# Kernel optimization log

Hardware: AMD Instinct MI355X
Metric: run time of the kernel (lower is better)

The kernel has to match this reference:

```python
import jax, jax.numpy as jnp
import numpy as np

N_NODES = 50000
NEG_SLOPE = 0.2  # PyG GATConv default leaky-relu slope


def _gat_conv(x, edge_index, W, a_src, a_dst, bias, heads, out_ch, concat, num_nodes):
    # x: [N, F_in]; W: [F_in, heads*out_ch]; a_src/a_dst: [heads, out_ch]; bias: [heads*out_ch] or [out_ch]
    h = (x @ W).reshape(num_nodes, heads, out_ch)            # [N,H,C]
    alpha_src = jnp.einsum('nhc,hc->nh', h, a_src)           # [N,H]
    alpha_dst = jnp.einsum('nhc,hc->nh', h, a_dst)           # [N,H]
    src, dst = edge_index[0], edge_index[1]
    e = jax.nn.leaky_relu(alpha_src[src] + alpha_dst[dst], NEG_SLOPE)  # [E,H]
    # segment softmax over incoming edges per destination (self-loops guarantee non-empty segments)
    m = jax.ops.segment_max(e, dst, num_segments=num_nodes)
    e = jnp.exp(e - m[dst])
    denom = jax.ops.segment_sum(e, dst, num_segments=num_nodes)
    alpha = e / denom[dst]                                    # [E,H]
    msg = h[src] * alpha[:, :, None]                          # [E,H,C]
    out = jax.ops.segment_sum(msg, dst, num_segments=num_nodes)  # [N,H,C]
    if concat:
        out = out.reshape(num_nodes, heads * out_ch)
    else:
        out = out.mean(axis=1)
    return out + bias


def _add_self_loops(edge_index, num_nodes):
    loops = jnp.arange(num_nodes, dtype=edge_index.dtype)
    return jnp.concatenate([edge_index, jnp.stack([loops, loops])], axis=1)


def setup_inputs() -> dict:
    key = jax.random.key(0)
    ks = jax.random.split(key, 16)
    N, F_in, H, C_hid, C_out = N_NODES, 128, 4, 64, 64
    E = 800000
    x = jax.random.normal(ks[0], (N, F_in), dtype=jnp.float32)
    edge_index = jax.random.randint(ks[1], (2, E), 0, N, dtype=jnp.int32)
    s = lambda fan: 1.0 / np.sqrt(fan)
    inp = {
        'x': x, 'edge_index': edge_index,
        'W1': jax.random.normal(ks[2], (F_in, H * C_hid), jnp.float32) * s(F_in),
        'a_src1': jax.random.normal(ks[3], (H, C_hid), jnp.float32) * s(C_hid),
        'a_dst1': jax.random.normal(ks[4], (H, C_hid), jnp.float32) * s(C_hid),
        'b1': jnp.zeros((H * C_hid,), jnp.float32),
        'W2': jax.random.normal(ks[5], (H * C_hid, H * C_hid), jnp.float32) * s(H * C_hid),
        'a_src2': jax.random.normal(ks[6], (H, C_hid), jnp.float32) * s(C_hid),
        'a_dst2': jax.random.normal(ks[7], (H, C_hid), jnp.float32) * s(C_hid),
        'b2': jnp.zeros((H * C_hid,), jnp.float32),
        'W3': jax.random.normal(ks[8], (H * C_hid, C_out), jnp.float32) * s(H * C_hid),
        'a_src3': jax.random.normal(ks[9], (1, C_out), jnp.float32) * s(C_out),
        'a_dst3': jax.random.normal(ks[10], (1, C_out), jnp.float32) * s(C_out),
        'b3': jnp.zeros((C_out,), jnp.float32),
    }
    return inp


def reference(x, edge_index, W1, a_src1, a_dst1, b1, W2, a_src2, a_dst2, b2, W3, a_src3, a_dst3, b3):
    N = x.shape[0]
    ei = _add_self_loops(edge_index, N)
    h = _gat_conv(x, ei, W1, a_src1, a_dst1, b1, heads=4, out_ch=64, concat=True, num_nodes=N)
    h = jax.nn.elu(h)
    h = _gat_conv(h, ei, W2, a_src2, a_dst2, b2, heads=4, out_ch=64, concat=True, num_nodes=N)
    h = jax.nn.elu(h)
    out = _gat_conv(h, ei, W3, a_src3, a_dst3, b3, heads=1, out_ch=64, concat=False, num_nodes=N)
    return out
```

## Files before the change

### kernel.cpp

```cpp
#include <hip/hip_runtime.h>
#include <hip/hip_fp16.h>
#include <cstdint>


typedef _Float16 f16;
typedef _Float16 f16x8 __attribute__((ext_vector_type(8)));
typedef float f32x4 __attribute__((ext_vector_type(4)));

__global__ __launch_bounds__(256) void count_kernel(const int* __restrict__ ei,
                                                    int E, int N,
                                                    int* __restrict__ deg) {
  int g = blockIdx.x * 256 + threadIdx.x;
  if (g >= E + N) return;
  int dst = (g < E) ? ei[E + g] : (g - E);
  atomicAdd(&deg[dst], 1);
}

__global__ __launch_bounds__(256) void deg_block_reduce(const int* __restrict__ deg,
                                                        int* __restrict__ bsum, int N) {
  __shared__ int red[4];
  int b = blockIdx.x;
  int v = 0;
#pragma unroll
  for (int s = 0; s < 4; ++s) {
    int idx = b * 1024 + s * 256 + threadIdx.x;
    if (idx < N) v += deg[idx];
  }
  for (int off = 32; off; off >>= 1) v += __shfl_down(v, off);
  if ((threadIdx.x & 63) == 0) red[threadIdx.x >> 6] = v;
  __syncthreads();
  if (threadIdx.x == 0) bsum[b] = red[0] + red[1] + red[2] + red[3];
}

__global__ __launch_bounds__(1024) void small_scan(const int* __restrict__ bsum,
                                                   int* __restrict__ bpre, int NB) {
  __shared__ int buf[1024];
  int v = (threadIdx.x < NB) ? bsum[threadIdx.x] : 0;
  buf[threadIdx.x] = v;
  __syncthreads();
  for (int off = 1; off < 1024; off <<= 1) {
    int tv = (threadIdx.x >= off) ? buf[threadIdx.x - off] : 0;
    __syncthreads();
    buf[threadIdx.x] += tv;
    __syncthreads();
  }
  if (threadIdx.x < NB) bpre[threadIdx.x] = buf[threadIdx.x] - v;
}

__global__ __launch_bounds__(1024) void scan_final(const int* __restrict__ deg,
                                                   const int* __restrict__ bpre,
                                                   int* __restrict__ row_off,
                                                   int* __restrict__ cursor,
                                                   int N, int total) {
  __shared__ int buf[1024];
  int b = blockIdx.x;
  int i = b * 1024 + threadIdx.x;
  int v = (i < N) ? deg[i] : 0;
  buf[threadIdx.x] = v;
  __syncthreads();
  for (int off = 1; off < 1024; off <<= 1) {
    int tv = (threadIdx.x >= off) ? buf[threadIdx.x - off] : 0;
    __syncthreads();
    buf[threadIdx.x] += tv;
    __syncthreads();
  }
  if (i < N) {
    int ro = bpre[b] + buf[threadIdx.x] - v;
    row_off[i] = ro;
    cursor[i] = ro;
  }
  if (i == 0) row_off[N] = total;
}

__global__ __launch_bounds__(256) void scatter_kernel(const int* __restrict__ ei,
                                                      int E, int N,
                                                      int* __restrict__ cursor,
                                                      int* __restrict__ esrc,
                                                      int* __restrict__ edst) {
  int g = blockIdx.x * 256 + threadIdx.x;
  if (g >= E + N) return;
  int src, dst;
  if (g < E) { src = ei[g]; dst = ei[E + g]; }
  else       { src = g - E; dst = src; }
  int pos = atomicAdd(&cursor[dst], 1);
  esrc[pos] = src;
  edst[pos] = dst;
}

__global__ __launch_bounds__(256) void convert_x(const float* __restrict__ x,
                                                 f16* __restrict__ xh, int n) {
  int i = (blockIdx.x * 256 + threadIdx.x) * 4;
  if (i >= n) return;
  float4 v = *reinterpret_cast<const float4*>(&x[i]);
  f16 o[4] = {(f16)v.x, (f16)v.y, (f16)v.z, (f16)v.w};
  *reinterpret_cast<uint2*>(&xh[i]) = *reinterpret_cast<uint2*>(o);
}

__global__ __launch_bounds__(256) void convert_wt(const float* __restrict__ W,
                                                  f16* __restrict__ Wt,
                                                  int K, int Ncol) {
  int t = blockIdx.x * 256 + threadIdx.x;
  if (t >= K * Ncol) return;
  int n = t % Ncol, k = t / Ncol;
  Wt[(size_t)n * K + k] = (f16)W[t];
}

template <int BN>
__global__ __launch_bounds__(256) void mfma_gemm_alpha(
    const f16* __restrict__ A,
    const f16* __restrict__ Bt,
    f16* __restrict__ Tout,
    const float* __restrict__ avec_src, const float* __restrict__ avec_dst,
    float* __restrict__ asrc, float* __restrict__ adst,
    int M, int K, int Ncol) {
  constexpr int CF = BN / 16;
  constexpr int HL = BN / 64;
  __shared__ f16 As[128][40];
  __shared__ f16 Bs[BN][40];
  int tid = threadIdx.x;
  int wv = tid >> 6, lane = tid & 63;
  int lrow = lane & 15, lkb = lane >> 4;
  int row0 = blockIdx.x * 128, col0 = blockIdx.y * BN;

  f32x4 acc[2][CF];
#pragma unroll
  for (int rf = 0; rf < 2; ++rf)
#pragma unroll
    for (int cf = 0; cf < CF; ++cf) acc[rf][cf] = (f32x4){0.f, 0.f, 0.f, 0.f};

  for (int kk = 0; kk < K; kk += 32) {
#pragma unroll
    for (int q = 0; q < 2; ++q) {
      int slot = tid + q * 256;
      int r = slot >> 2, ko = (slot & 3) << 3;
      int gr = min(row0 + r, M - 1);
      *reinterpret_cast<f16x8*>(&As[r][ko]) =
          *reinterpret_cast<const f16x8*>(&A[(size_t)gr * K + kk + ko]);
    }
#pragma unroll
    for (int q = 0; q < BN / 64; ++q) {
      int slot = tid + q * 256;
      int c = slot >> 2, ko = (slot & 3) << 3;
      *reinterpret_cast<f16x8*>(&Bs[c][ko]) =
          *reinterpret_cast<const f16x8*>(&Bt[(size_t)(col0 + c) * K + kk + ko]);
    }
    __syncthreads();
    f16x8 af[2], bf[CF];
#pragma unroll
    for (int rf = 0; rf < 2; ++rf)
      af[rf] = *reinterpret_cast<f16x8*>(&As[wv * 32 + rf * 16 + lrow][lkb * 8]);
#pragma unroll
    for (int cf = 0; cf < CF; ++cf)
      bf[cf] = *reinterpret_cast<f16x8*>(&Bs[cf * 16 + lrow][lkb * 8]);
#pragma unroll
    for (int rf = 0; rf < 2; ++rf)
#pragma unroll
      for (int cf = 0; cf < CF; ++cf)
        acc[rf][cf] = __builtin_amdgcn_mfma_f32_16x16x32_f16(af[rf], bf[cf],
                                                             acc[rf][cf], 0, 0, 0);
    __syncthreads();
  }

  int Hh = Ncol >> 6;
  float avs[HL][4], avd[HL][4];
#pragma unroll
  for (int hl = 0; hl < HL; ++hl) {
    int hg = (col0 >> 6) + hl;
#pragma unroll
    for (int q = 0; q < 4; ++q) {
      avs[hl][q] = avec_src[hg * 64 + q * 16 + lrow];
      avd[hl][q] = avec_dst[hg * 64 + q * 16 + lrow];
    }
  }

#pragma unroll
  for (int rf = 0; rf < 2; ++rf) {
#pragma unroll
    for (int hl = 0; hl < HL; ++hl) {
      int hg = (col0 >> 6) + hl;
#pragma unroll
      for (int r = 0; r < 4; ++r) {
        float ps = 0.f, pd = 0.f;
#pragma unroll
        for (int q = 0; q < 4; ++q) {
          float v = acc[rf][hl * 4 + q][r];
          ps = fmaf(v, avs[hl][q], ps);
          pd = fmaf(v, avd[hl][q], pd);
        }
#pragma unroll
        for (int off = 1; off < 16; off <<= 1) {
          ps += __shfl_xor(ps, off);
          pd += __shfl_xor(pd, off);
        }
        int row = row0 + wv * 32 + rf * 16 + lkb * 4 + r;
        if (lrow == 0 && row < M) {
          asrc[row * Hh + hg] = ps;
          adst[row * Hh + hg] = pd;
        }
      }
    }
#pragma unroll
    for (int r = 0; r < 4; ++r) {
      int row = row0 + wv * 32 + rf * 16 + lkb * 4 + r;
      if (row < M) {
#pragma unroll
        for (int cf = 0; cf < CF; ++cf)
          Tout[(size_t)row * Ncol + col0 + cf * 16 + lrow] = (f16)acc[rf][cf][r];
      }
    }
  }
}

__global__ __launch_bounds__(256) void edge_weights_h4(
    const int* __restrict__ esrc, const int* __restrict__ edst,
    const float* __restrict__ asrc, const float* __restrict__ adst,
    float* __restrict__ w, int ET) {
  int t = blockIdx.x * 256 + threadIdx.x;
  if (t >= ET * 4) return;
  int j = t >> 2, h = t & 3;
  float e = asrc[esrc[j] * 4 + h] + adst[edst[j] * 4 + h];
  e = fmaxf(e, 0.2f * e);
  w[t] = __expf(e);
}

__global__ __launch_bounds__(256) void edge_weights_h1(
    const int* __restrict__ esrc, const int* __restrict__ edst,
    const float* __restrict__ asrc, const float* __restrict__ adst,
    float* __restrict__ w, int ET) {
  int j = blockIdx.x * 256 + threadIdx.x;
  if (j >= ET) return;
  float e = asrc[esrc[j]] + adst[edst[j]];
  e = fmaxf(e, 0.2f * e);
  w[j] = __expf(e);
}

template <bool ELU>
__global__ __launch_bounds__(256) void aggregate_h4(
    const f16* __restrict__ T16, const int* __restrict__ row_off,
    const int* __restrict__ esrc, const float* __restrict__ w,
    const float* __restrict__ bias, f16* __restrict__ outF, int N) {
  int wv = threadIdx.x >> 6, lane = threadIdx.x & 63;
  int dst = blockIdx.x * 4 + wv;
  if (dst >= N) return;
  int head = lane >> 4;
  int r0 = row_off[dst], r1 = row_off[dst + 1];
  const char* tbase = reinterpret_cast<const char*>(T16);
  uint loff = (uint)lane * 8;
  float den = 0.f, ax = 0.f, ay = 0.f, az = 0.f, aw = 0.f;
#pragma unroll 2
  for (int j = r0; j < r1; ++j) {
    int sj = esrc[j];
    float wj = w[(j << 2) + head];
    den += wj;
    uint2 raw = *reinterpret_cast<const uint2*>(tbase + (((uint)sj << 9) + loff));
    __half2 p0 = *reinterpret_cast<__half2*>(&raw.x);
    __half2 p1 = *reinterpret_cast<__half2*>(&raw.y);
    float2 f0 = __half22float2(p0);
    float2 f1 = __half22float2(p1);
    ax = fmaf(wj, f0.x, ax);
    ay = fmaf(wj, f0.y, ay);
    az = fmaf(wj, f1.x, az);
    aw = fmaf(wj, f1.y, aw);
  }
  float rd = 1.f / den;
  float4 bv = *reinterpret_cast<const float4*>(&bias[lane << 2]);
  float vx = ax * rd + bv.x, vy = ay * rd + bv.y;
  float vz = az * rd + bv.z, vw = aw * rd + bv.w;
  if (ELU) {
    vx = vx > 0.f ? vx : expm1f(vx);
    vy = vy > 0.f ? vy : expm1f(vy);
    vz = vz > 0.f ? vz : expm1f(vz);
    vw = vw > 0.f ? vw : expm1f(vw);
  }
  f16 o[4] = {(f16)vx, (f16)vy, (f16)vz, (f16)vw};
  *reinterpret_cast<uint2*>(&outF[(size_t)dst * 256 + (lane << 2)]) =
      *reinterpret_cast<uint2*>(o);
}

__global__ __launch_bounds__(256) void aggregate_h1(
    const f16* __restrict__ T16, const int* __restrict__ row_off,
    const int* __restrict__ esrc, const float* __restrict__ w,
    const float* __restrict__ bias, float* __restrict__ out, int N) {
  int wv = threadIdx.x >> 6, lane = threadIdx.x & 63;
  int g = lane >> 4, l = lane & 15;
  int dst = blockIdx.x * 4 + wv;
  if (dst >= N) return;
  int r0 = row_off[dst], r1 = row_off[dst + 1];
  const char* tbase = reinterpret_cast<const char*>(T16);
  uint coff = (uint)l * 8;
  float den = 0.f, ax = 0.f, ay = 0.f, az = 0.f, aw = 0.f;
#pragma unroll 2
  for (int j = r0 + g; j < r1; j += 4) {
    int sj = esrc[j];
    float wj = w[j];
    den += wj;
    uint2 raw = *reinterpret_cast<const uint2*>(tbase + (((uint)sj << 7) + coff));
    __half2 p0 = *reinterpret_cast<__half2*>(&raw.x);
    __half2 p1 = *reinterpret_cast<__half2*>(&raw.y);
    float2 f0 = __half22float2(p0);
    float2 f1 = __half22float2(p1);
    ax = fmaf(wj, f0.x, ax);
    ay = fmaf(wj, f0.y, ay);
    az = fmaf(wj, f1.x, az);
    aw = fmaf(wj, f1.y, aw);
  }
#pragma unroll
  for (int off = 16; off < 64; off <<= 1) {
    ax += __shfl_xor(ax, off);
    ay += __shfl_xor(ay, off);
    az += __shfl_xor(az, off);
    aw += __shfl_xor(aw, off);
    den += __shfl_xor(den, off);
  }
  if (lane < 16) {
    float rd = 1.f / den;
    float4 v;
    v.x = ax * rd + bias[l * 4 + 0];
    v.y = ay * rd + bias[l * 4 + 1];
    v.z = az * rd + bias[l * 4 + 2];
    v.w = aw * rd + bias[l * 4 + 3];
    *reinterpret_cast<float4*>(&out[(size_t)dst * 64 + l * 4]) = v;
  }
}

extern "C" void kernel_launch(void* const* d_in, const int* in_sizes, int n_in,
                              void* d_out, int out_size, void* d_ws, size_t ws_size,
                              hipStream_t stream) {
  const float* x   = (const float*)d_in[0];
  const int*   ei  = (const int*)d_in[1];
  const float* W1  = (const float*)d_in[2];
  const float* as1 = (const float*)d_in[3];
  const float* ad1 = (const float*)d_in[4];
  const float* b1  = (const float*)d_in[5];
  const float* W2  = (const float*)d_in[6];
  const float* as2 = (const float*)d_in[7];
  const float* ad2 = (const float*)d_in[8];
  const float* b2  = (const float*)d_in[9];
  const float* W3  = (const float*)d_in[10];
  const float* as3 = (const float*)d_in[11];
  const float* ad3 = (const float*)d_in[12];
  const float* b3  = (const float*)d_in[13];
  float* out = (float*)d_out;

  const int Fin = 128, H = 4, C = 64, HC = H * C;
  const int N = in_sizes[0] / Fin;
  const int E = in_sizes[1] / 2;
  const int ET = E + N;
  const int NB = (N + 1023) / 1024;

  f16* xh    = (f16*)d_ws;
  f16* T16   = xh + (size_t)N * Fin;
  f16* F16   = T16 + (size_t)N * HC;
  f16* T16L3 = F16 + (size_t)N * HC;
  f16* Wt1   = T16L3 + (size_t)N * C;
  f16* Wt2   = Wt1 + HC * Fin;
  f16* Wt3   = Wt2 + HC * HC;
  float* asrc = (float*)(Wt3 + C * HC);
  float* adst = asrc + (size_t)N * H;
  float* wbuf = adst + (size_t)N * H;
  int* deg     = (int*)(wbuf + (size_t)ET * 4);
  int* row_off = deg + N;
  int* cursor  = row_off + (N + 1);
  int* bsum    = cursor + N;
  int* bpre    = bsum + NB;
  int* esrc    = bpre + NB;
  int* edst    = esrc + ET;

  hipMemsetAsync(deg, 0, N * sizeof(int), stream);
  count_kernel<<<(ET + 255) / 256, 256, 0, stream>>>(ei, E, N, deg);
  deg_block_reduce<<<NB, 256, 0, stream>>>(deg, bsum, N);
  small_scan<<<1, 1024, 0, stream>>>(bsum, bpre, NB);
  scan_final<<<NB, 1024, 0, stream>>>(deg, bpre, row_off, cursor, N, ET);
  scatter_kernel<<<(ET + 255) / 256, 256, 0, stream>>>(ei, E, N, cursor, esrc, edst);

  convert_x<<<(N * Fin / 4 + 255) / 256, 256, 0, stream>>>(x, xh, N * Fin);
  convert_wt<<<(Fin * HC + 255) / 256, 256, 0, stream>>>(W1, Wt1, Fin, HC);
  convert_wt<<<(HC * HC + 255) / 256, 256, 0, stream>>>(W2, Wt2, HC, HC);
  convert_wt<<<(HC * C + 255) / 256, 256, 0, stream>>>(W3, Wt3, HC, C);

  int gx = (N + 127) / 128;
  int eb4 = (ET * 4 + 255) / 256, eb1 = (ET + 255) / 256;
  int ab = (N + 3) / 4;

  mfma_gemm_alpha<128><<<dim3(gx, 2), 256, 0, stream>>>(
      xh, Wt1, T16, as1, ad1, asrc, adst, N, Fin, HC);
  edge_weights_h4<<<eb4, 256, 0, stream>>>(esrc, edst, asrc, adst, wbuf, ET);
  aggregate_h4<true><<<ab, 256, 0, stream>>>(T16, row_off, esrc, wbuf, b1, F16, N);

  mfma_gemm_alpha<128><<<dim3(gx, 2), 256, 0, stream>>>(
      F16, Wt2, T16, as2, ad2, asrc, adst, N, HC, HC);
  edge_weights_h4<<<eb4, 256, 0, stream>>>(esrc, edst, asrc, adst, wbuf, ET);
  aggregate_h4<true><<<ab, 256, 0, stream>>>(T16, row_off, esrc, wbuf, b2, F16, N);

  mfma_gemm_alpha<64><<<dim3(gx, 1), 256, 0, stream>>>(
      F16, Wt3, T16L3, as3, ad3, asrc, adst, N, HC, C);
  edge_weights_h1<<<eb1, 256, 0, stream>>>(esrc, edst, asrc, adst, wbuf, ET);
  aggregate_h1<<<ab, 256, 0, stream>>>(T16L3, row_off, esrc, wbuf, b3, out, N);
}
```

Before: 367.2 us.

## Slice feature matrices into 32-column panels and aggregate per slice

GEMM outputs and aggregation outputs now use a column-sliced layout: 32-wide f16 panels, each stored contiguously over all nodes. The aggregation kernel runs one block per slice and node chunk, with 8 lanes per edge row and 8 edges in flight per wave. The aim is a smaller gather footprint per pass so it stays in L2/cache, plus more memory-level parallelism per destination. Edge weights are computed once per edge with float4 loads and stored head-major. The cost is that edge indices and weights are re-read once per slice, adding index traffic.

New measurement: 518.0 us. +41.1%, slower.

```diff
diff --git a/kernel.cpp b/kernel.cpp
--- a/kernel.cpp
+++ b/kernel.cpp
@@ -105,10 +105,9 @@
   Wt[(size_t)n * K + k] = (f16)W[t];
 }
 
-template <int BN>
+template <int BN, bool ASL>
 __global__ __launch_bounds__(256) void mfma_gemm_alpha(
-    const f16* __restrict__ A,
-    const f16* __restrict__ Bt,
+    const f16* __restrict__ A, const f16* __restrict__ Bt,
     f16* __restrict__ Tout,
     const float* __restrict__ avec_src, const float* __restrict__ avec_dst,
     float* __restrict__ asrc, float* __restrict__ adst,
@@ -121,6 +120,7 @@
   int wv = tid >> 6, lane = tid & 63;
   int lrow = lane & 15, lkb = lane >> 4;
   int row0 = blockIdx.x * 128, col0 = blockIdx.y * BN;
+  size_t Msl = (size_t)M * 32;
 
   f32x4 acc[2][CF];
 #pragma unroll
@@ -134,8 +134,9 @@
       int slot = tid + q * 256;
       int r = slot >> 2, ko = (slot & 3) << 3;
       int gr = min(row0 + r, M - 1);
-      *reinterpret_cast<f16x8*>(&As[r][ko]) =
-          *reinterpret_cast<const f16x8*>(&A[(size_t)gr * K + kk + ko]);
+      const f16* Ap = ASL ? &A[(size_t)(kk >> 5) * Msl + (size_t)gr * 32 + ko]
+                          : &A[(size_t)gr * K + kk + ko];
+      *reinterpret_cast<f16x8*>(&As[r][ko]) = *reinterpret_cast<const f16x8*>(Ap);
     }
 #pragma unroll
     for (int q = 0; q < BN / 64; ++q) {
@@ -204,8 +205,11 @@
       int row = row0 + wv * 32 + rf * 16 + lkb * 4 + r;
       if (row < M) {
 #pragma unroll
-        for (int cf = 0; cf < CF; ++cf)
-          Tout[(size_t)row * Ncol + col0 + cf * 16 + lrow] = (f16)acc[rf][cf][r];
+        for (int cf = 0; cf < CF; ++cf) {
+          int col = col0 + cf * 16 + lrow;
+          Tout[(size_t)(col >> 5) * Msl + (size_t)row * 32 + (col & 31)] =
+              (f16)acc[rf][cf][r];
+        }
       }
     }
   }
@@ -215,12 +219,18 @@
     const int* __restrict__ esrc, const int* __restrict__ edst,
     const float* __restrict__ asrc, const float* __restrict__ adst,
     float* __restrict__ w, int ET) {
-  int t = blockIdx.x * 256 + threadIdx.x;
-  if (t >= ET * 4) return;
-  int j = t >> 2, h = t & 3;
-  float e = asrc[esrc[j] * 4 + h] + adst[edst[j] * 4 + h];
-  e = fmaxf(e, 0.2f * e);
-  w[t] = __expf(e);
+  int j = blockIdx.x * 256 + threadIdx.x;
+  if (j >= ET) return;
+  float4 s4 = *reinterpret_cast<const float4*>(&asrc[esrc[j] * 4]);
+  float4 d4 = *reinterpret_cast<const float4*>(&adst[edst[j] * 4]);
+  float e0 = s4.x + d4.x; e0 = fmaxf(e0, 0.2f * e0);
+  float e1 = s4.y + d4.y; e1 = fmaxf(e1, 0.2f * e1);
+  float e2 = s4.z + d4.z; e2 = fmaxf(e2, 0.2f * e2);
+  float e3 = s4.w + d4.w; e3 = fmaxf(e3, 0.2f * e3);
+  w[j] = __expf(e0);
+  w[ET + j] = __expf(e1);
+  w[2 * ET + j] = __expf(e2);
+  w[3 * ET + j] = __expf(e3);
 }
 
 __global__ __launch_bounds__(256) void edge_weights_h1(
@@ -234,92 +244,70 @@
   w[j] = __expf(e);
 }
 
-template <bool ELU>
-__global__ __launch_bounds__(256) void aggregate_h4(
-    const f16* __restrict__ T16, const int* __restrict__ row_off,
-    const int* __restrict__ esrc, const float* __restrict__ w,
-    const float* __restrict__ bias, f16* __restrict__ outF, int N) {
+template <int NSL, bool ELU, bool F32OUT>
+__global__ __launch_bounds__(256) void aggregate_sliced(
+    const f16* __restrict__ Tsl,
+    const int* __restrict__ row_off, const int* __restrict__ esrc,
+    const float* __restrict__ w,
+    const float* __restrict__ bias, void* __restrict__ outp,
+    int N, int ET) {
+  int s = blockIdx.x % NSL;
+  int chunk = blockIdx.x / NSL;
   int wv = threadIdx.x >> 6, lane = threadIdx.x & 63;
-  int dst = blockIdx.x * 4 + wv;
-  if (dst >= N) return;
-  int head = lane >> 4;
-  int r0 = row_off[dst], r1 = row_off[dst + 1];
-  const char* tbase = reinterpret_cast<const char*>(T16);
-  uint loff = (uint)lane * 8;
-  float den = 0.f, ax = 0.f, ay = 0.f, az = 0.f, aw = 0.f;
-#pragma unroll 2
-  for (int j = r0; j < r1; ++j) {
-    int sj = esrc[j];
-    float wj = w[(j << 2) + head];
-    den += wj;
-    uint2 raw = *reinterpret_cast<const uint2*>(tbase + (((uint)sj << 9) + loff));
-    __half2 p0 = *reinterpret_cast<__half2*>(&raw.x);
-    __half2 p1 = *reinterpret_cast<__half2*>(&raw.y);
-    float2 f0 = __half22float2(p0);
-    float2 f1 = __half22float2(p1);
-    ax = fmaf(wj, f0.x, ax);
-    ay = fmaf(wj, f0.y, ay);
-    az = fmaf(wj, f1.x, az);
-    aw = fmaf(wj, f1.y, aw);
-  }
-  float rd = 1.f / den;
-  float4 bv = *reinterpret_cast<const float4*>(&bias[lane << 2]);
-  float vx = ax * rd + bv.x, vy = ay * rd + bv.y;
-  float vz = az * rd + bv.z, vw = aw * rd + bv.w;
-  if (ELU) {
-    vx = vx > 0.f ? vx : expm1f(vx);
-    vy = vy > 0.f ? vy : expm1f(vy);
-    vz = vz > 0.f ? vz : expm1f(vz);
-    vw = vw > 0.f ? vw : expm1f(vw);
-  }
-  f16 o[4] = {(f16)vx, (f16)vy, (f16)vz, (f16)vw};
-  *reinterpret_cast<uint2*>(&outF[(size_t)dst * 256 + (lane << 2)]) =
-      *reinterpret_cast<uint2*>(o);
-}
-
-__global__ __launch_bounds__(256) void aggregate_h1(
-    const f16* __restrict__ T16, const int* __restrict__ row_off,
-    const int* __restrict__ esrc, const float* __restrict__ w,
-    const float* __restrict__ bias, float* __restrict__ out, int N) {
-  int wv = threadIdx.x >> 6, lane = threadIdx.x & 63;
-  int g = lane >> 4, l = lane & 15;
-  int dst = blockIdx.x * 4 + wv;
-  if (dst >= N) return;
-  int r0 = row_off[dst], r1 = row_off[dst + 1];
-  const char* tbase = reinterpret_cast<const char*>(T16);
-  uint coff = (uint)l * 8;
-  float den = 0.f, ax = 0.f, ay = 0.f, az = 0.f, aw = 0.f;
-#pragma unroll 2
-  for (int j = r0 + g; j < r1; j += 4) {
-    int sj = esrc[j];
-    float wj = w[j];
-    den += wj;
-    uint2 raw = *reinterpret_cast<const uint2*>(tbase + (((uint)sj << 7) + coff));
-    __half2 p0 = *reinterpret_cast<__half2*>(&raw.x);
-    __half2 p1 = *reinterpret_cast<__half2*>(&raw.y);
-    float2 f0 = __half22float2(p0);
-    float2 f1 = __half22float2(p1);
-    ax = fmaf(wj, f0.x, ax);
-    ay = fmaf(wj, f0.y, ay);
-    az = fmaf(wj, f1.x, az);
-    aw = fmaf(wj, f1.y, aw);
-  }
-#pragma unroll
-  for (int off = 16; off < 64; off <<= 1) {
-    ax += __shfl_xor(ax, off);
-    ay += __shfl_xor(ay, off);
-    az += __shfl_xor(az, off);
-    aw += __shfl_xor(aw, off);
-    den += __shfl_xor(den, off);
-  }
-  if (lane < 16) {
-    float rd = 1.f / den;
-    float4 v;
-    v.x = ax * rd + bias[l * 4 + 0];
-    v.y = ay * rd + bias[l * 4 + 1];
-    v.z = az * rd + bias[l * 4 + 2];
-    v.w = aw * rd + bias[l * 4 + 3];
-    *reinterpret_cast<float4*>(&out[(size_t)dst * 64 + l * 4]) = v;
+  int g = lane >> 3, l = lane & 7;
+  int head = s >> 1;
+  const f16* tb = Tsl + (size_t)s * N * 32;
+  const float* wh = w + (size_t)head * ET;
+  int dbase = chunk * 16 + wv * 4;
+#pragma unroll
+  for (int d = 0; d < 4; ++d) {
+    int dst = dbase + d;
+    if (dst >= N) return;
+    int r0 = row_off[dst], r1 = row_off[dst + 1];
+    float den = 0.f, ax = 0.f, ay = 0.f, az = 0.f, aw = 0.f;
+    for (int j = r0 + g; j < r1; j += 8) {
+      int sj = esrc[j];
+      float wj = wh[j];
+      den += wj;
+      uint2 raw = *reinterpret_cast<const uint2*>(tb + (size_t)sj * 32 + l * 4);
+      __half2 p0 = *reinterpret_cast<__half2*>(&raw.x);
+      __half2 p1 = *reinterpret_cast<__half2*>(&raw.y);
+      float2 f0 = __half22float2(p0);
+      float2 f1 = __half22float2(p1);
+      ax = fmaf(wj, f0.x, ax);
+      ay = fmaf(wj, f0.y, ay);
+      az = fmaf(wj, f1.x, az);
+      aw = fmaf(wj, f1.y, aw);
+    }
+#pragma unroll
+    for (int off = 8; off < 64; off <<= 1) {
+      ax += __shfl_xor(ax, off);
+      ay += __shfl_xor(ay, off);
+      az += __shfl_xor(az, off);
+      aw += __shfl_xor(aw, off);
+      den += __shfl_xor(den, off);
+    }
+    if (lane < 8) {
+      float rd = 1.f / den;
+      int c0 = s * 32 + l * 4;
+      float4 bv = *reinterpret_cast<const float4*>(&bias[c0]);
+      float vx = ax * rd + bv.x, vy = ay * rd + bv.y;
+      float vz = az * rd + bv.z, vw = aw * rd + bv.w;
+      if (ELU) {
+        vx = vx > 0.f ? vx : expm1f(vx);
+        vy = vy > 0.f ? vy : expm1f(vy);
+        vz = vz > 0.f ? vz : expm1f(vz);
+        vw = vw > 0.f ? vw : expm1f(vw);
+      }
+      if (F32OUT) {
+        *reinterpret_cast<float4*>((float*)outp + (size_t)dst * (NSL * 32) + c0) =
+            make_float4(vx, vy, vz, vw);
+      } else {
+        f16 o[4] = {(f16)vx, (f16)vy, (f16)vz, (f16)vw};
+        *reinterpret_cast<uint2*>((f16*)outp + ((size_t)s * N + dst) * 32 + l * 4) =
+            *reinterpret_cast<uint2*>(o);
+      }
+    }
   }
 }
 
@@ -379,21 +367,25 @@
   convert_wt<<<(HC * C + 255) / 256, 256, 0, stream>>>(W3, Wt3, HC, C);
 
   int gx = (N + 127) / 128;
-  int eb4 = (ET * 4 + 255) / 256, eb1 = (ET + 255) / 256;
-  int ab = (N + 3) / 4;
-
-  mfma_gemm_alpha<128><<<dim3(gx, 2), 256, 0, stream>>>(
+  int eb = (ET + 255) / 256;
+  int agg4 = 8 * ((N + 15) / 16);
+  int agg1 = 2 * ((N + 15) / 16);
+
+  mfma_gemm_alpha<128, false><<<dim3(gx, 2), 256, 0, stream>>>(
       xh, Wt1, T16, as1, ad1, asrc, adst, N, Fin, HC);
-  edge_weights_h4<<<eb4, 256, 0, stream>>>(esrc, edst, asrc, adst, wbuf, ET);
-  aggregate_h4<true><<<ab, 256, 0, stream>>>(T16, row_off, esrc, wbuf, b1, F16, N);
-
-  mfma_gemm_alpha<128><<<dim3(gx, 2), 256, 0, stream>>>(
+  edge_weights_h4<<<eb, 256, 0, stream>>>(esrc, edst, asrc, adst, wbuf, ET);
+  aggregate_sliced<8, true, false><<<agg4, 256, 0, stream>>>(
+      T16, row_off, esrc, wbuf, b1, F16, N, ET);
+
+  mfma_gemm_alpha<128, true><<<dim3(gx, 2), 256, 0, stream>>>(
       F16, Wt2, T16, as2, ad2, asrc, adst, N, HC, HC);
-  edge_weights_h4<<<eb4, 256, 0, stream>>>(esrc, edst, asrc, adst, wbuf, ET);
-  aggregate_h4<true><<<ab, 256, 0, stream>>>(T16, row_off, esrc, wbuf, b2, F16, N);
-
-  mfma_gemm_alpha<64><<<dim3(gx, 1), 256, 0, stream>>>(
+  edge_weights_h4<<<eb, 256, 0, stream>>>(esrc, edst, asrc, adst, wbuf, ET);
+  aggregate_sliced<8, true, false><<<agg4, 256, 0, stream>>>(
+      T16, row_off, esrc, wbuf, b2, F16, N, ET);
+
+  mfma_gemm_alpha<64, true><<<dim3(gx, 1), 256, 0, stream>>>(
       F16, Wt3, T16L3, as3, ad3, asrc, adst, N, HC, C);
-  edge_weights_h1<<<eb1, 256, 0, stream>>>(esrc, edst, asrc, adst, wbuf, ET);
-  aggregate_h1<<<ab, 256, 0, stream>>>(T16L3, row_off, esrc, wbuf, b3, out, N);
-}
+  edge_weights_h1<<<eb, 256, 0, stream>>>(esrc, edst, asrc, adst, wbuf, ET);
+  aggregate_sliced<2, false, true><<<agg1, 256, 0, stream>>>(
+      T16L3, row_off, esrc, wbuf, b3, out, N, ET);
+}
```

## Batch edge index/weight loads via wave shuffles and give each 16-lane group its own node in layer 3

Applied to the files above, without the earlier changes.

In the 4-head aggregation, each group of 8 edges now has its source indices and weights loaded cooperatively by separate lanes and broadcast with shuffles. The old loop issued the same scalar loads from every lane for every edge. The 1-head aggregation is restructured so each 16-lane group handles its own destination node instead of four groups splitting one node's edges. This removes the cross-group shuffle reduction and uses four times fewer blocks. The trade-offs are padded zero-weight iterations on nodes whose degree is not a multiple of 8, and possible load imbalance between groups within a wave.

New measurement: 337.2 us. 1.09x faster.

```diff
diff --git a/kernel.cpp b/kernel.cpp
--- a/kernel.cpp
+++ b/kernel.cpp
@@ -107,8 +107,7 @@
 
 template <int BN>
 __global__ __launch_bounds__(256) void mfma_gemm_alpha(
-    const f16* __restrict__ A,
-    const f16* __restrict__ Bt,
+    const f16* __restrict__ A, const f16* __restrict__ Bt,
     f16* __restrict__ Tout,
     const float* __restrict__ avec_src, const float* __restrict__ avec_dst,
     float* __restrict__ asrc, float* __restrict__ adst,
@@ -243,24 +242,34 @@
   int dst = blockIdx.x * 4 + wv;
   if (dst >= N) return;
   int head = lane >> 4;
+  int hsel = lane & 48;
   int r0 = row_off[dst], r1 = row_off[dst + 1];
   const char* tbase = reinterpret_cast<const char*>(T16);
   uint loff = (uint)lane * 8;
   float den = 0.f, ax = 0.f, ay = 0.f, az = 0.f, aw = 0.f;
-#pragma unroll 2
-  for (int j = r0; j < r1; ++j) {
-    int sj = esrc[j];
-    float wj = w[(j << 2) + head];
-    den += wj;
-    uint2 raw = *reinterpret_cast<const uint2*>(tbase + (((uint)sj << 9) + loff));
-    __half2 p0 = *reinterpret_cast<__half2*>(&raw.x);
-    __half2 p1 = *reinterpret_cast<__half2*>(&raw.y);
-    float2 f0 = __half22float2(p0);
-    float2 f1 = __half22float2(p1);
-    ax = fmaf(wj, f0.x, ax);
-    ay = fmaf(wj, f0.y, ay);
-    az = fmaf(wj, f1.x, az);
-    aw = fmaf(wj, f1.y, aw);
+  for (int base = r0; base < r1; base += 8) {
+    int jb = base + (lane & 7);
+    int sv = 0;
+    float wl = 0.f;
+    if (jb < r1) {
+      sv = esrc[jb];
+      wl = w[(jb << 2) + head];
+    }
+#pragma unroll
+    for (int i = 0; i < 8; ++i) {
+      int sj = __shfl(sv, i);
+      float wj = __shfl(wl, hsel + i);
+      den += wj;
+      uint2 raw = *reinterpret_cast<const uint2*>(tbase + (((uint)sj << 9) + loff));
+      __half2 p0 = *reinterpret_cast<__half2*>(&raw.x);
+      __half2 p1 = *reinterpret_cast<__half2*>(&raw.y);
+      float2 f0 = __half22float2(p0);
+      float2 f1 = __half22float2(p1);
+      ax = fmaf(wj, f0.x, ax);
+      ay = fmaf(wj, f0.y, ay);
+      az = fmaf(wj, f1.x, az);
+      aw = fmaf(wj, f1.y, aw);
+    }
   }
   float rd = 1.f / den;
   float4 bv = *reinterpret_cast<const float4*>(&bias[lane << 2]);
@@ -282,45 +291,45 @@
     const int* __restrict__ esrc, const float* __restrict__ w,
     const float* __restrict__ bias, float* __restrict__ out, int N) {
   int wv = threadIdx.x >> 6, lane = threadIdx.x & 63;
-  int g = lane >> 4, l = lane & 15;
-  int dst = blockIdx.x * 4 + wv;
+  int grp = lane >> 4, l = lane & 15;
+  int gsel = lane & 48;
+  int dst = blockIdx.x * 16 + wv * 4 + grp;
   if (dst >= N) return;
   int r0 = row_off[dst], r1 = row_off[dst + 1];
   const char* tbase = reinterpret_cast<const char*>(T16);
-  uint coff = (uint)l * 8;
+  uint loff = (uint)l * 8;
   float den = 0.f, ax = 0.f, ay = 0.f, az = 0.f, aw = 0.f;
-#pragma unroll 2
-  for (int j = r0 + g; j < r1; j += 4) {
-    int sj = esrc[j];
-    float wj = w[j];
-    den += wj;
-    uint2 raw = *reinterpret_cast<const uint2*>(tbase + (((uint)sj << 7) + coff));
-    __half2 p0 = *reinterpret_cast<__half2*>(&raw.x);
-    __half2 p1 = *reinterpret_cast<__half2*>(&raw.y);
-    float2 f0 = __half22float2(p0);
-    float2 f1 = __half22float2(p1);
-    ax = fmaf(wj, f0.x, ax);
-    ay = fmaf(wj, f0.y, ay);
-    az = fmaf(wj, f1.x, az);
-    aw = fmaf(wj, f1.y, aw);
-  }
-#pragma unroll
-  for (int off = 16; off < 64; off <<= 1) {
-    ax += __shfl_xor(ax, off);
-    ay += __shfl_xor(ay, off);
-    az += __shfl_xor(az, off);
-    aw += __shfl_xor(aw, off);
-    den += __shfl_xor(den, off);
-  }
-  if (lane < 16) {
-    float rd = 1.f / den;
-    float4 v;
-    v.x = ax * rd + bias[l * 4 + 0];
-    v.y = ay * rd + bias[l * 4 + 1];
-    v.z = az * rd + bias[l * 4 + 2];
-    v.w = aw * rd + bias[l * 4 + 3];
-    *reinterpret_cast<float4*>(&out[(size_t)dst * 64 + l * 4]) = v;
-  }
+  for (int base = r0; base < r1; base += 8) {
+    int jb = base + (l & 7);
+    int sv = 0;
+    float wl = 0.f;
+    if (jb < r1) {
+      sv = esrc[jb];
+      wl = w[jb];
+    }
+#pragma unroll
+    for (int i = 0; i < 8; ++i) {
+      int sj = __shfl(sv, gsel + i);
+      float wj = __shfl(wl, gsel + i);
+      den += wj;
+      uint2 raw = *reinterpret_cast<const uint2*>(tbase + (((uint)sj << 7) + loff));
+      __half2 p0 = *reinterpret_cast<__half2*>(&raw.x);
+      __half2 p1 = *reinterpret_cast<__half2*>(&raw.y);
+      float2 f0 = __half22float2(p0);
+      float2 f1 = __half22float2(p1);
+      ax = fmaf(wj, f0.x, ax);
+      ay = fmaf(wj, f0.y, ay);
+      az = fmaf(wj, f1.x, az);
+      aw = fmaf(wj, f1.y, aw);
+    }
+  }
+  float rd = 1.f / den;
+  float4 v;
+  v.x = ax * rd + bias[l * 4 + 0];
+  v.y = ay * rd + bias[l * 4 + 1];
+  v.z = az * rd + bias[l * 4 + 2];
+  v.w = aw * rd + bias[l * 4 + 3];
+  *reinterpret_cast<float4*>(&out[(size_t)dst * 64 + l * 4]) = v;
 }
 
 extern "C" void kernel_launch(void* const* d_in, const int* in_sizes, int n_in,
@@ -380,20 +389,21 @@
 
   int gx = (N + 127) / 128;
   int eb4 = (ET * 4 + 255) / 256, eb1 = (ET + 255) / 256;
-  int ab = (N + 3) / 4;
+  int ab4 = (N + 3) / 4;
+  int ab1 = (N + 15) / 16;
 
   mfma_gemm_alpha<128><<<dim3(gx, 2), 256, 0, stream>>>(
       xh, Wt1, T16, as1, ad1, asrc, adst, N, Fin, HC);
   edge_weights_h4<<<eb4, 256, 0, stream>>>(esrc, edst, asrc, adst, wbuf, ET);
-  aggregate_h4<true><<<ab, 256, 0, stream>>>(T16, row_off, esrc, wbuf, b1, F16, N);
+  aggregate_h4<true><<<ab4, 256, 0, stream>>>(T16, row_off, esrc, wbuf, b1, F16, N);
 
   mfma_gemm_alpha<128><<<dim3(gx, 2), 256, 0, stream>>>(
       F16, Wt2, T16, as2, ad2, asrc, adst, N, HC, HC);
   edge_weights_h4<<<eb4, 256, 0, stream>>>(esrc, edst, asrc, adst, wbuf, ET);
-  aggregate_h4<true><<<ab, 256, 0, stream>>>(T16, row_off, esrc, wbuf, b2, F16, N);
+  aggregate_h4<true><<<ab4, 256, 0, stream>>>(T16, row_off, esrc, wbuf, b2, F16, N);
 
   mfma_gemm_alpha<64><<<dim3(gx, 1), 256, 0, stream>>>(
       F16, Wt3, T16L3, as3, ad3, asrc, adst, N, HC, C);
   edge_weights_h1<<<eb1, 256, 0, stream>>>(esrc, edst, asrc, adst, wbuf, ET);
-  aggregate_h1<<<ab, 256, 0, stream>>>(T16L3, row_off, esrc, wbuf, b3, out, N);
-}
+  aggregate_h1<<<ab1, 256, 0, stream>>>(T16L3, row_off, esrc, wbuf, b3, out, N);
+}
```
